# Kernel optimization log

Measured on AMD Instinct MI355X. Metric: run time of the kernel, lower is better.

The kernel has to match this reference:

```python
import jax, jax.numpy as jnp
import numpy as np

NUM_HEADS = 16
HEAD_DIM = 64  # 1024 / 16


def setup_inputs() -> dict:
    key = jax.random.key(0)
    ks = jax.random.split(key, 8)
    B, S, D = 2, 2048, 1024
    s = 0.02
    return {
        "hidden_states_q": jax.random.normal(ks[0], (B, S, D), jnp.float32),
        "hidden_states_k": jax.random.normal(ks[1], (B, S, D), jnp.float32),
        "hidden_states_v": jax.random.normal(ks[2], (B, S, D), jnp.float32),
        "Wq": jax.random.normal(ks[3], (D, D), jnp.float32) * s,
        "bq": jnp.zeros((D,), jnp.float32),
        "Wk": jax.random.normal(ks[4], (D, D), jnp.float32) * s,
        "bk": jnp.zeros((D,), jnp.float32),
        "Wv": jax.random.normal(ks[5], (D, D), jnp.float32) * s,
        "bv": jnp.zeros((D,), jnp.float32),
        "Wp": jax.random.normal(ks[6], (D, D), jnp.float32) * s,
        "bp": jnp.zeros((D,), jnp.float32),
    }


def _split_heads(x):
    B, S, D = x.shape
    return x.reshape(B, S, NUM_HEADS, HEAD_DIM).transpose(0, 2, 1, 3)  # [B,H,S,dh]


def reference(hidden_states_q, hidden_states_k, hidden_states_v,
              Wq, bq, Wk, bk, Wv, bv, Wp, bp):
    # Projections (Linear / Conv1D are both x @ W + b in this parameterization)
    q = _split_heads(hidden_states_q @ Wq + bq)
    k = _split_heads(hidden_states_k @ Wk + bk)
    v = _split_heads(hidden_states_v @ Wv + bv)
    scale = 1.0 / jnp.sqrt(jnp.asarray(HEAD_DIM, q.dtype))
    # NOTE: no causal mask is applied in the original _attn (mask asserted None)
    attn = jnp.einsum("bhqd,bhkd->bhqk", q, k) * scale
    attn = jax.nn.softmax(attn, axis=-1)  # attn_dropout is identity in eval
    out = jnp.einsum("bhqk,bhkd->bhqd", attn, v)
    B, H, S, dh = out.shape
    out = out.transpose(0, 2, 1, 3).reshape(B, S, H * dh)
    out = out @ Wp + bp  # resid_dropout identity in eval
    return out
```

## Files before the change

kernel.cpp:

```cpp
#include <hip/hip_runtime.h>
#include <stdint.h>


typedef _Float16 f16;
typedef __attribute__((ext_vector_type(8))) _Float16 f16x8;
typedef __attribute__((ext_vector_type(4))) _Float16 f16x4;
typedef __attribute__((ext_vector_type(2))) _Float16 f16x2;
typedef __attribute__((ext_vector_type(4))) float f32x4;
typedef __attribute__((ext_vector_type(16))) float f32x16;
typedef __attribute__((ext_vector_type(2))) unsigned u32x2;

#define NB 2
#define SEQ 2048
#define DMODEL 1024
#define NH 16
#define DH 64

#define QSCALE 0.1803368801111601f

__device__ __forceinline__ void gload_lds16(const void* g, void* l) {
  __builtin_amdgcn_global_load_lds(
      (const __attribute__((address_space(1))) unsigned int*)g,
      (__attribute__((address_space(3))) unsigned int*)l, 16, 0, 0);
}

__device__ __forceinline__ void plswap(unsigned& a, unsigned& b) {
  u32x2 r = __builtin_amdgcn_permlane32_swap(a, b, false, false);
  a = r[0];
  b = r[1];
}

__global__ __launch_bounds__(256) void prep(
    const float* __restrict__ hq, const float* __restrict__ hk,
    const float* __restrict__ hv, f16* __restrict__ xq, f16* __restrict__ xk,
    f16* __restrict__ xv, const float* __restrict__ w0,
    const float* __restrict__ w1, const float* __restrict__ w2,
    const float* __restrict__ w3, f16* __restrict__ t0, f16* __restrict__ t1,
    f16* __restrict__ t2, f16* __restrict__ t3) {
  __shared__ float tile[64][65];
  const int z = blockIdx.z;
  if (z < 3) {
    const float* src = z == 0 ? hq : (z == 1 ? hk : hv);
    f16* dst = z == 0 ? xq : (z == 1 ? xk : xv);
    int i = (blockIdx.x * 256 + threadIdx.x) * 8;
    float4 a = *(const float4*)(src + i);
    float4 b = *(const float4*)(src + i + 4);
    f16x8 o;
    o[0] = (f16)a.x; o[1] = (f16)a.y; o[2] = (f16)a.z; o[3] = (f16)a.w;
    o[4] = (f16)b.x; o[5] = (f16)b.y; o[6] = (f16)b.z; o[7] = (f16)b.w;
    *(f16x8*)(dst + i) = o;
    return;
  }
  if (blockIdx.x >= 256) return;
  const float* W; f16* T;
  switch (z - 3) {
    case 0: W = w0; T = t0; break;
    case 1: W = w1; T = t1; break;
    case 2: W = w2; T = t2; break;
    default: W = w3; T = t3; break;
  }
  int r0 = (blockIdx.x >> 4) * 64, c0 = (blockIdx.x & 15) * 64;
  for (int it = 0; it < 16; ++it) {
    int idx = it * 256 + threadIdx.x;
    int r = idx >> 6, c = idx & 63;
    tile[r][c] = W[(size_t)(r0 + r) * DMODEL + c0 + c];
  }
  __syncthreads();
  for (int it = 0; it < 16; ++it) {
    int idx = it * 256 + threadIdx.x;
    int r = idx >> 6, c = idx & 63;
    T[(size_t)(c0 + r) * DMODEL + r0 + c] = (f16)tile[c][r];
  }
}

__global__ __launch_bounds__(256) void gemm128(
    const f16* __restrict__ xq, const f16* __restrict__ xk,
    const f16* __restrict__ xv,
    const f16* __restrict__ wqt, const f16* __restrict__ wkt,
    const f16* __restrict__ wvt,
    const float* __restrict__ bq, const float* __restrict__ bk,
    const float* __restrict__ bv,
    f16* __restrict__ qo, f16* __restrict__ ko, f16* __restrict__ vto) {
  __shared__ char lds[32768];
  char* ldsA = lds;
  char* ldsB = lds + 16384;

  const int bid = blockIdx.x;
  const int mode = bid >> 8;
  const int lin = bid & 255;
  const int m0 = ((lin & 7) + 8 * ((lin >> 3) & 3)) * 128;
  const int n0 = (lin >> 5) * 128;

  const f16* Am; const f16* Bt; const float* bias; float oscale = 1.0f;
  if (mode == 0)      { Am = xq; Bt = wqt; bias = bq; oscale = QSCALE; }
  else if (mode == 1) { Am = xk; Bt = wkt; bias = bk; }
  else                { Am = xv; Bt = wvt; bias = bv; }

  const int tid = threadIdx.x;
  const int l = tid & 63, w = tid >> 6;
  const int g = l >> 4, c = l & 15;
  const int wr = w >> 1, wc = w & 1;

  const int srow = w * 8 + (l >> 3);
  const int schunk = (l & 7) ^ ((l >> 3) & 7);

  f32x4 acc[4][4] = {};

  for (int k0 = 0; k0 < DMODEL; k0 += 64) {
#pragma unroll
    for (int it = 0; it < 4; ++it) {
      int row = it * 32 + srow;
      gload_lds16(Am + (size_t)(m0 + row) * DMODEL + k0 + schunk * 8,
                  ldsA + it * 4096 + w * 1024);
    }
#pragma unroll
    for (int it = 0; it < 4; ++it) {
      int row = it * 32 + srow;
      gload_lds16(Bt + (size_t)(n0 + row) * DMODEL + k0 + schunk * 8,
                  ldsB + it * 4096 + w * 1024);
    }
    __syncthreads();
    f16x8 af[2][4], bf[2][4];
#pragma unroll
    for (int kc = 0; kc < 2; ++kc)
#pragma unroll
      for (int i = 0; i < 4; ++i) {
        int row = wr * 64 + i * 16 + c;
        af[kc][i] = *(const f16x8*)(ldsA + row * 128 + (((kc * 4 + g) ^ (row & 7)) << 4));
        int rowb = wc * 64 + i * 16 + c;
        bf[kc][i] = *(const f16x8*)(ldsB + rowb * 128 + (((kc * 4 + g) ^ (rowb & 7)) << 4));
      }
#pragma unroll
    for (int kc = 0; kc < 2; ++kc)
#pragma unroll
      for (int i = 0; i < 4; ++i)
#pragma unroll
        for (int j = 0; j < 4; ++j)
          acc[i][j] = __builtin_amdgcn_mfma_f32_16x16x32_f16(af[kc][i], bf[kc][j],
                                                             acc[i][j], 0, 0, 0);
    __syncthreads();
  }

#pragma unroll
  for (int i = 0; i < 4; ++i) {
#pragma unroll
    for (int j = 0; j < 4; ++j) {
      int grb = m0 + wr * 64 + i * 16 + g * 4;
      int gc = n0 + wc * 64 + j * 16 + c;
      float bval = bias[gc];
      if (mode == 2) {
        int b = grb >> 11, s = grb & 2047, h = gc >> 6, d = gc & 63;
        f16x4 pk;
#pragma unroll
        for (int e = 0; e < 4; ++e) pk[e] = (f16)(acc[i][j][e] + bval);
        *(f16x4*)(vto + ((size_t)((b * NH + h) * DH + d)) * SEQ + s) = pk;
      } else {
        f16* dst = (mode == 0) ? qo : ko;
        int b = grb >> 11, s = grb & 2047, h = gc >> 6, d = gc & 63;
#pragma unroll
        for (int e = 0; e < 4; ++e)
          dst[(((size_t)(b * NH + h) * SEQ) + (s + e)) * DH + d] =
              (f16)((acc[i][j][e] + bval) * oscale);
      }
    }
  }
}

__global__ __launch_bounds__(256) void gemm_out(
    const f16* __restrict__ ao, const f16* __restrict__ wpt,
    const float* __restrict__ bp, float* __restrict__ out) {
  __shared__ char lds[24576];
  char* ldsA = lds;
  char* ldsB = lds + 16384;

  const int lin = blockIdx.x;
  const int m0 = ((lin & 7) + 8 * ((lin >> 3) & 3)) * 128;
  const int n0 = (lin >> 5) * 64;

  const int tid = threadIdx.x;
  const int l = tid & 63, w = tid >> 6;
  const int g = l >> 4, c = l & 15;
  const int wr = w >> 1, wc = w & 1;

  const int srow = w * 8 + (l >> 3);
  const int schunk = (l & 7) ^ ((l >> 3) & 7);

  f32x4 acc[4][2] = {};

  for (int k0 = 0; k0 < DMODEL; k0 += 64) {
#pragma unroll
    for (int it = 0; it < 4; ++it) {
      int row = it * 32 + srow;
      gload_lds16(ao + (size_t)(m0 + row) * DMODEL + k0 + schunk * 8,
                  ldsA + it * 4096 + w * 1024);
    }
#pragma unroll
    for (int it = 0; it < 2; ++it) {
      int row = it * 32 + srow;
      gload_lds16(wpt + (size_t)(n0 + row) * DMODEL + k0 + schunk * 8,
                  ldsB + it * 4096 + w * 1024);
    }
    __syncthreads();
    f16x8 af[2][4], bf[2][2];
#pragma unroll
    for (int kc = 0; kc < 2; ++kc) {
#pragma unroll
      for (int i = 0; i < 4; ++i) {
        int row = wr * 64 + i * 16 + c;
        af[kc][i] = *(const f16x8*)(ldsA + row * 128 + (((kc * 4 + g) ^ (row & 7)) << 4));
      }
#pragma unroll
      for (int j = 0; j < 2; ++j) {
        int rowb = wc * 32 + j * 16 + c;
        bf[kc][j] = *(const f16x8*)(ldsB + rowb * 128 + (((kc * 4 + g) ^ (rowb & 7)) << 4));
      }
    }
#pragma unroll
    for (int kc = 0; kc < 2; ++kc)
#pragma unroll
      for (int i = 0; i < 4; ++i)
#pragma unroll
        for (int j = 0; j < 2; ++j)
          acc[i][j] = __builtin_amdgcn_mfma_f32_16x16x32_f16(af[kc][i], bf[kc][j],
                                                             acc[i][j], 0, 0, 0);
    __syncthreads();
  }

#pragma unroll
  for (int i = 0; i < 4; ++i)
#pragma unroll
    for (int j = 0; j < 2; ++j) {
      int grb = m0 + wr * 64 + i * 16 + g * 4;
      int gc = n0 + wc * 32 + j * 16 + c;
      float bval = bp[gc];
#pragma unroll
      for (int e = 0; e < 4; ++e)
        out[(size_t)(grb + e) * DMODEL + gc] = acc[i][j][e] + bval;
    }
}

__global__ __launch_bounds__(256, 2) void attn64(
    const f16* __restrict__ qg, const f16* __restrict__ kg,
    const f16* __restrict__ vtg, f16* __restrict__ aout) {
  __shared__ char lds[65536];

  const int tid = threadIdx.x;
  const int l = tid & 63, w = tid >> 6;
  const int q31 = l & 31;
  const bool hi = l >= 32;
  const int p = w & 1;
  const int qgrp = w >> 1;

  const int bid = blockIdx.x;
  const int bh = (bid & 7) + 8 * (bid >> 7);
  const int qc = (bid >> 3) & 15;
  const int q0 = qc * 128 + qgrp * 64;

  f16x8 qf0[4], qf1[4];
#pragma unroll
  for (int ks = 0; ks < 4; ++ks) {
    qf0[ks] = *(const f16x8*)(qg + ((size_t)bh * SEQ + q0 + q31) * DH + ks * 16 +
                              (hi ? 8 : 0));
    qf1[ks] = *(const f16x8*)(qg + ((size_t)bh * SEQ + q0 + 32 + q31) * DH +
                              ks * 16 + (hi ? 8 : 0));
  }

  float lsum0 = 0.0f, lsum1 = 0.0f;
  f32x16 oacc00 = {}, oacc01 = {}, oacc10 = {}, oacc11 = {};

  const int srow = w * 8 + (l >> 3);
  const int schunk = (l & 7) ^ ((l >> 3) & 7);

  auto stage = [&](int buf, int t) {
    char* baseK = lds + buf * 16384;
    char* baseV = baseK + 8192;
#pragma unroll
    for (int it = 0; it < 2; ++it) {
      int row = it * 32 + srow;
      gload_lds16(kg + ((size_t)bh * SEQ + t * 64 + row) * DH + schunk * 8,
                  baseK + it * 4096 + w * 1024);
      gload_lds16(vtg + ((size_t)bh * DH + row) * SEQ + t * 64 + schunk * 8,
                  baseV + it * 4096 + w * 1024);
    }
  };

  const f16x2 one2 = {(f16)1.0f, (f16)1.0f};

  auto softmax = [&](const f32x16& st, float& lsum, unsigned* dw) {
    float ps[16];
#pragma unroll
    for (int r = 0; r < 16; ++r) ps[r] = exp2f(st[r]);
#pragma unroll
    for (int i = 0; i < 8; ++i)
      dw[i] = __builtin_bit_cast(
          unsigned, __builtin_amdgcn_cvt_pkrtz(ps[2 * i], ps[2 * i + 1]));
    float sA = 0.0f, sB = 0.0f;
#pragma unroll
    for (int i = 0; i < 4; ++i) {
      sA = __builtin_amdgcn_fdot2(__builtin_bit_cast(f16x2, dw[i]), one2, sA, false);
      sB = __builtin_amdgcn_fdot2(__builtin_bit_cast(f16x2, dw[4 + i]), one2, sB, false);
    }
    lsum += sA + sB;
    plswap(dw[0], dw[2]);
    plswap(dw[1], dw[3]);
    plswap(dw[4], dw[6]);
    plswap(dw[5], dw[7]);
  };

  auto compute = [&](const char* ldsK) {
    const char* ldsV = ldsK + 8192;
    f32x16 st0 = {}, st1 = {};
#pragma unroll
    for (int ks = 0; ks < 4; ++ks) {
      int row = p * 32 + q31;
      int ch = ((ks * 2 + (hi ? 1 : 0)) ^ (q31 & 7)) << 4;
      f16x8 kf = *(const f16x8*)(ldsK + row * 128 + ch);
      st0 = __builtin_amdgcn_mfma_f32_32x32x16_f16(kf, qf0[ks], st0, 0, 0, 0);
      st1 = __builtin_amdgcn_mfma_f32_32x32x16_f16(kf, qf1[ks], st1, 0, 0, 0);
    }
    unsigned dw0[8], dw1[8];
    softmax(st0, lsum0, dw0);
    softmax(st1, lsum1, dw1);
#pragma unroll
    for (int ks2 = 0; ks2 < 2; ++ks2) {
      union { unsigned u[4]; f16x8 v; } pb0, pb1;
      pb0.u[0] = dw0[ks2 * 4 + 0]; pb0.u[1] = dw0[ks2 * 4 + 1];
      pb0.u[2] = dw0[ks2 * 4 + 2]; pb0.u[3] = dw0[ks2 * 4 + 3];
      pb1.u[0] = dw1[ks2 * 4 + 0]; pb1.u[1] = dw1[ks2 * 4 + 1];
      pb1.u[2] = dw1[ks2 * 4 + 2]; pb1.u[3] = dw1[ks2 * 4 + 3];
      {
        int vrow = q31;
        int ch = ((p * 4 + ks2 * 2 + (hi ? 1 : 0)) ^ (vrow & 7)) << 4;
        f16x8 vf = *(const f16x8*)(ldsV + vrow * 128 + ch);
        oacc00 = __builtin_amdgcn_mfma_f32_32x32x16_f16(vf, pb0.v, oacc00, 0, 0, 0);
        oacc10 = __builtin_amdgcn_mfma_f32_32x32x16_f16(vf, pb1.v, oacc10, 0, 0, 0);
      }
      {
        int vrow = 32 + q31;
        int ch = ((p * 4 + ks2 * 2 + (hi ? 1 : 0)) ^ (vrow & 7)) << 4;
        f16x8 vf = *(const f16x8*)(ldsV + vrow * 128 + ch);
        oacc01 = __builtin_amdgcn_mfma_f32_32x32x16_f16(vf, pb0.v, oacc01, 0, 0, 0);
        oacc11 = __builtin_amdgcn_mfma_f32_32x32x16_f16(vf, pb1.v, oacc11, 0, 0, 0);
      }
    }
  };

  stage(0, 0);
  stage(1, 1);

#pragma unroll 2
  for (int tt = 0; tt < 32; tt += 2) {
    asm volatile("s_waitcnt vmcnt(0)" ::: "memory");
    __builtin_amdgcn_s_barrier();
    __builtin_amdgcn_sched_barrier(0);
    if (tt + 2 < 32) {
      stage((tt + 2) & 3, tt + 2);
      stage((tt + 3) & 3, tt + 3);
    }
    compute(lds + (tt & 3) * 16384);
    compute(lds + ((tt + 1) & 3) * 16384);
  }

  __syncthreads();
  char* reg = lds + qgrp * 16896;
  if (p == 1) {
#pragma unroll
    for (int j = 0; j < 8; ++j) {
      f32x4 c0, c1;
#pragma unroll
      for (int e = 0; e < 4; ++e) {
        c0[e] = (j < 4) ? oacc00[j * 4 + e] : oacc01[(j - 4) * 4 + e];
        c1[e] = (j < 4) ? oacc10[j * 4 + e] : oacc11[(j - 4) * 4 + e];
      }
      *(f32x4*)(reg + j * 1024 + l * 16) = c0;
      *(f32x4*)(reg + 8192 + j * 1024 + l * 16) = c1;
    }
    *(float*)(reg + 16384 + l * 4) = lsum0;
    *(float*)(reg + 16640 + l * 4) = lsum1;
  }
  __syncthreads();
  if (p == 0) {
#pragma unroll
    for (int j = 0; j < 8; ++j) {
      f32x4 c0 = *(const f32x4*)(reg + j * 1024 + l * 16);
      f32x4 c1 = *(const f32x4*)(reg + 8192 + j * 1024 + l * 16);
#pragma unroll
      for (int e = 0; e < 4; ++e) {
        if (j < 4) { oacc00[j * 4 + e] += c0[e]; oacc10[j * 4 + e] += c1[e]; }
        else       { oacc01[(j - 4) * 4 + e] += c0[e]; oacc11[(j - 4) * 4 + e] += c1[e]; }
      }
    }
    float lt0 = lsum0 + *(const float*)(reg + 16384 + l * 4);
    float lt1 = lsum1 + *(const float*)(reg + 16640 + l * 4);
    lt0 += __shfl_xor(lt0, 32);
    lt1 += __shfl_xor(lt1, 32);
    float inv0 = 1.0f / lt0, inv1 = 1.0f / lt1;
    const int b = bh >> 4, h = bh & 15;
#pragma unroll
    for (int f = 0; f < 2; ++f) {
      float inv = f ? inv1 : inv0;
      int s = q0 + f * 32 + q31;
#pragma unroll
      for (int dt = 0; dt < 2; ++dt)
#pragma unroll
        for (int rg = 0; rg < 4; ++rg) {
          f16x4 pk;
#pragma unroll
          for (int j = 0; j < 4; ++j) {
            float v = f ? (dt ? oacc11[rg * 4 + j] : oacc10[rg * 4 + j])
                        : (dt ? oacc01[rg * 4 + j] : oacc00[rg * 4 + j]);
            pk[j] = (f16)(v * inv);
          }
          int d0 = dt * 32 + rg * 8 + (hi ? 4 : 0);
          *(f16x4*)(aout + ((size_t)(b * SEQ + s)) * DMODEL + h * DH + d0) = pk;
        }
    }
  }
}

extern "C" void kernel_launch(void* const* d_in, const int* in_sizes, int n_in,
                              void* d_out, int out_size, void* d_ws, size_t ws_size,
                              hipStream_t stream) {
  const float* hq = (const float*)d_in[0];
  const float* hk = (const float*)d_in[1];
  const float* hv = (const float*)d_in[2];
  const float* Wq = (const float*)d_in[3];
  const float* bq = (const float*)d_in[4];
  const float* Wk = (const float*)d_in[5];
  const float* bk = (const float*)d_in[6];
  const float* Wv = (const float*)d_in[7];
  const float* bv = (const float*)d_in[8];
  const float* Wp = (const float*)d_in[9];
  const float* bp = (const float*)d_in[10];
  float* out = (float*)d_out;

  f16* xq  = (f16*)d_ws;
  f16* xk  = xq + 4194304;
  f16* xv  = xk + 4194304;
  f16* wqt = xv + 4194304;
  f16* wkt = wqt + 1048576;
  f16* wvt = wkt + 1048576;
  f16* wpt = wvt + 1048576;
  f16* qb  = wpt + 1048576;
  f16* kb  = qb + 4194304;
  f16* vtb = kb + 4194304;
  f16* ao  = vtb + 4194304;

  prep<<<dim3(2048, 1, 7), 256, 0, stream>>>(hq, hk, hv, xq, xk, xv,
                                             Wq, Wk, Wv, Wp, wqt, wkt, wvt, wpt);
  gemm128<<<dim3(768), 256, 0, stream>>>(xq, xk, xv, wqt, wkt, wvt,
                                         bq, bk, bv, qb, kb, vtb);
  attn64<<<dim3(512), 256, 0, stream>>>(qb, kb, vtb, ao);
  gemm_out<<<dim3(512), 256, 0, stream>>>(ao, wpt, bp, out);
}
```

Before: 130.9 us.

## Give each wave private K/V LDS slices and drop per-tile block barriers

Each wave now stages only the K rows and V^T columns for its own 32-key half into a private LDS region, double-buffered, instead of staging full shared 64-key tiles for the whole block. Because no wave reads another wave's data, the block-wide s_barrier is removed and each wave waits only on its own loads with a partial vmcnt. This cuts synchronization stalls and lets waves drift independently. In exchange, waves in the same query group redundantly fetch the same K/V halves, which raises global traffic, and the pipeline depth drops from two tiles ahead to one.

```diff
diff --git a/kernel.cpp b/kernel.cpp
--- a/kernel.cpp
+++ b/kernel.cpp
@@ -268,19 +268,22 @@
   float lsum0 = 0.0f, lsum1 = 0.0f;
   f32x16 oacc00 = {}, oacc01 = {}, oacc10 = {}, oacc11 = {};
 
-  const int srow = w * 8 + (l >> 3);
-  const int schunk = (l & 7) ^ ((l >> 3) & 7);
+  char* ldsW = lds + w * 16384;
+
+  const int skK = (l & 7) ^ ((l >> 3) & 7);
+  const int skV = (l & 3) ^ ((l >> 3) & 3);
 
   auto stage = [&](int buf, int t) {
-    char* baseK = lds + buf * 16384;
-    char* baseV = baseK + 8192;
-#pragma unroll
-    for (int it = 0; it < 2; ++it) {
-      int row = it * 32 + srow;
-      gload_lds16(kg + ((size_t)bh * SEQ + t * 64 + row) * DH + schunk * 8,
-                  baseK + it * 4096 + w * 1024);
-      gload_lds16(vtg + ((size_t)bh * DH + row) * SEQ + t * 64 + schunk * 8,
-                  baseV + it * 4096 + w * 1024);
+    char* baseK = ldsW + buf * 8192;
+    char* baseV = baseK + 4096;
+#pragma unroll
+    for (int it = 0; it < 4; ++it) {
+      gload_lds16(kg + ((size_t)bh * SEQ + t * 64 + p * 32 + it * 8 + (l >> 3)) * DH +
+                      skK * 8,
+                  baseK + it * 1024);
+      gload_lds16(vtg + ((size_t)bh * DH + it * 16 + (l >> 2)) * SEQ + t * 64 +
+                      p * 32 + skV * 8,
+                  baseV + it * 1024);
     }
   };
 
@@ -308,13 +311,12 @@
   };
 
   auto compute = [&](const char* ldsK) {
-    const char* ldsV = ldsK + 8192;
+    const char* ldsV = ldsK + 4096;
     f32x16 st0 = {}, st1 = {};
 #pragma unroll
     for (int ks = 0; ks < 4; ++ks) {
-      int row = p * 32 + q31;
       int ch = ((ks * 2 + (hi ? 1 : 0)) ^ (q31 & 7)) << 4;
-      f16x8 kf = *(const f16x8*)(ldsK + row * 128 + ch);
+      f16x8 kf = *(const f16x8*)(ldsK + q31 * 128 + ch);
       st0 = __builtin_amdgcn_mfma_f32_32x32x16_f16(kf, qf0[ks], st0, 0, 0, 0);
       st1 = __builtin_amdgcn_mfma_f32_32x32x16_f16(kf, qf1[ks], st1, 0, 0, 0);
     }
@@ -328,37 +330,34 @@
       pb0.u[2] = dw0[ks2 * 4 + 2]; pb0.u[3] = dw0[ks2 * 4 + 3];
       pb1.u[0] = dw1[ks2 * 4 + 0]; pb1.u[1] = dw1[ks2 * 4 + 1];
       pb1.u[2] = dw1[ks2 * 4 + 2]; pb1.u[3] = dw1[ks2 * 4 + 3];
-      {
-        int vrow = q31;
-        int ch = ((p * 4 + ks2 * 2 + (hi ? 1 : 0)) ^ (vrow & 7)) << 4;
-        f16x8 vf = *(const f16x8*)(ldsV + vrow * 128 + ch);
-        oacc00 = __builtin_amdgcn_mfma_f32_32x32x16_f16(vf, pb0.v, oacc00, 0, 0, 0);
-        oacc10 = __builtin_amdgcn_mfma_f32_32x32x16_f16(vf, pb1.v, oacc10, 0, 0, 0);
-      }
-      {
-        int vrow = 32 + q31;
-        int ch = ((p * 4 + ks2 * 2 + (hi ? 1 : 0)) ^ (vrow & 7)) << 4;
-        f16x8 vf = *(const f16x8*)(ldsV + vrow * 128 + ch);
-        oacc01 = __builtin_amdgcn_mfma_f32_32x32x16_f16(vf, pb0.v, oacc01, 0, 0, 0);
-        oacc11 = __builtin_amdgcn_mfma_f32_32x32x16_f16(vf, pb1.v, oacc11, 0, 0, 0);
+#pragma unroll
+      for (int dt = 0; dt < 2; ++dt) {
+        int vrow = dt * 32 + q31;
+        int ch = ((ks2 * 2 + (hi ? 1 : 0)) ^ ((vrow >> 1) & 3)) << 4;
+        f16x8 vf = *(const f16x8*)(ldsV + vrow * 64 + ch);
+        if (dt == 0) {
+          oacc00 = __builtin_amdgcn_mfma_f32_32x32x16_f16(vf, pb0.v, oacc00, 0, 0, 0);
+          oacc10 = __builtin_amdgcn_mfma_f32_32x32x16_f16(vf, pb1.v, oacc10, 0, 0, 0);
+        } else {
+          oacc01 = __builtin_amdgcn_mfma_f32_32x32x16_f16(vf, pb0.v, oacc01, 0, 0, 0);
+          oacc11 = __builtin_amdgcn_mfma_f32_32x32x16_f16(vf, pb1.v, oacc11, 0, 0, 0);
+        }
       }
     }
   };
 
   stage(0, 0);
-  stage(1, 1);
 
 #pragma unroll 2
-  for (int tt = 0; tt < 32; tt += 2) {
-    asm volatile("s_waitcnt vmcnt(0)" ::: "memory");
-    __builtin_amdgcn_s_barrier();
+  for (int t = 0; t < 32; ++t) {
+    if (t + 1 < 32) {
+      stage((t + 1) & 1, t + 1);
+      asm volatile("s_waitcnt vmcnt(8)" ::: "memory");
+    } else {
+      asm volatile("s_waitcnt vmcnt(0)" ::: "memory");
+    }
     __builtin_amdgcn_sched_barrier(0);
-    if (tt + 2 < 32) {
-      stage((tt + 2) & 3, tt + 2);
-      stage((tt + 3) & 3, tt + 3);
-    }
-    compute(lds + (tt & 3) * 16384);
-    compute(lds + ((tt + 1) & 3) * 16384);
+    compute(ldsW + (t & 1) * 8192);
   }
 
   __syncthreads();
```

Result: no change. 131.4 us (+0.4%).
